# Performance work log

Measured on AMD Instinct MI355X. Metric: run time of the kernel, lower is better.

## Reference

```python
import jax, jax.numpy as jnp
import numpy as np

HIDDEN = 1024
N_HEAD = 16
D_HEAD = HIDDEN // N_HEAD


def setup_inputs() -> dict:
    key = jax.random.key(0)
    ks = jax.random.split(key, 12)
    B, S, H = 2, 2048, HIDDEN
    scale = 1.0 / np.sqrt(H)
    inp = {
        "q": jax.random.normal(ks[0], (B, S, H), jnp.float32),
        "k": jax.random.normal(ks[1], (B, S, H), jnp.float32),
        "v": jax.random.normal(ks[2], (B, S, H), jnp.float32),
        "mask": jnp.ones((B, 1, S, S), jnp.int32),
        "w_q": jax.random.normal(ks[3], (H, H), jnp.float32) * scale,
        "b_q": jnp.zeros((H,), jnp.float32),
        "w_k": jax.random.normal(ks[4], (H, H), jnp.float32) * scale,
        "b_k": jnp.zeros((H,), jnp.float32),
        "w_v": jax.random.normal(ks[5], (H, H), jnp.float32) * scale,
        "b_v": jnp.zeros((H,), jnp.float32),
        "w_o": jax.random.normal(ks[6], (H, H), jnp.float32) * scale,
        "b_o": jnp.zeros((H,), jnp.float32),
    }
    return inp


def reference(q, k, v, mask, w_q, b_q, w_k, b_k, w_v, b_v, w_o, b_o):
    B, Sq, H = q.shape
    Sk = k.shape[1]
    # projections (weights stored as [in, out])
    qh = (q @ w_q + b_q).reshape(B, Sq, N_HEAD, D_HEAD).transpose(0, 2, 1, 3)
    kh = (k @ w_k + b_k).reshape(B, Sk, N_HEAD, D_HEAD).transpose(0, 2, 1, 3)
    vh = (v @ w_v + b_v).reshape(B, Sk, N_HEAD, D_HEAD).transpose(0, 2, 1, 3)
    scores = jnp.einsum("bhqd,bhkd->bhqk", qh, kh) * (D_HEAD ** -0.5)
    scores = jnp.where(mask == 0, jnp.float32(-10000.0), scores)
    attn = jax.nn.softmax(scores, axis=-1)
    out = jnp.einsum("bhqk,bhkd->bhqd", attn, vh)
    out = out.transpose(0, 2, 1, 3).reshape(B, Sq, H)
    return out @ w_o + b_o
```

## Files before the change

kernel.cpp:

```cpp
#include <hip/hip_runtime.h>
#include <hip/hip_bf16.h>
#include <stdint.h>

#define S_LEN 2048
#define HID   1024
#define NHEAD 16
#define DHEAD 64
#define BATCH 2

#define QSCALE 0.18033688f
#define MASKNEG -14427.0f

typedef __bf16 bf16_t;
typedef __bf16 bf16x4 __attribute__((ext_vector_type(4)));
typedef __bf16 bf16x8 __attribute__((ext_vector_type(8)));
typedef float  f32x4  __attribute__((ext_vector_type(4)));


__device__ __forceinline__ void gl_lds16(const bf16_t* g, bf16_t* l) {
  __builtin_amdgcn_global_load_lds((const __attribute__((address_space(1))) void*)g,
                                   (__attribute__((address_space(3))) void*)l,
                                   16, 0, 0);
}

template<int TR, int TC>
__device__ __forceinline__ void stage_tile(const bf16_t* __restrict__ g, int ldg,
                                           bf16_t* lds, int wave, int lane) {
  constexpr int CH = TC / 8;
  constexpr int NINST = (TR * CH) / 64;
  #pragma unroll
  for (int i = wave; i < NINST; i += 4) {
    int slot = i * 64 + lane;
    int r  = slot / CH;
    int cs = slot & (CH - 1);
    int c  = cs ^ (r & (CH - 1));
    gl_lds16(g + (size_t)r * ldg + c * 8, lds + i * 512);
  }
}

template<int CH>
__device__ __forceinline__ bf16x8 frag_ld(const bf16_t* lds, int row, int kchunk) {
  int cs = kchunk ^ (row & (CH - 1));
  return *(const bf16x8*)(lds + (row * CH + cs) * 8);
}

__global__ __launch_bounds__(256) void cvt3(const float* __restrict__ q,
                                            const float* __restrict__ k,
                                            const float* __restrict__ v,
                                            bf16_t* __restrict__ qb,
                                            bf16_t* __restrict__ kb,
                                            bf16_t* __restrict__ vb) {
  int which = blockIdx.y;
  const float* src = which == 0 ? q : which == 1 ? k : v;
  bf16_t* dst = which == 0 ? qb : which == 1 ? kb : vb;
  size_t i = ((size_t)blockIdx.x * 256 + threadIdx.x) * 4;
  float4 u = *(const float4*)(src + i);
  bf16x4 o = {(bf16_t)u.x, (bf16_t)u.y, (bf16_t)u.z, (bf16_t)u.w};
  *(bf16x4*)(dst + i) = o;
}

__global__ __launch_bounds__(256) void transpose_w4(
    const float* __restrict__ w0, const float* __restrict__ w1,
    const float* __restrict__ w2, const float* __restrict__ w3,
    bf16_t* __restrict__ wt, int* __restrict__ flags) {
  if (blockIdx.x == 0 && blockIdx.y == 0 && blockIdx.z == 0) {
    flags[threadIdx.x] = -1;
    flags[threadIdx.x + 256] = -1;
  }
  __shared__ float t[64][65];
  const float* W = blockIdx.z == 0 ? w0 : blockIdx.z == 1 ? w1 : blockIdx.z == 2 ? w2 : w3;
  bf16_t* WT = wt + (size_t)blockIdx.z * HID * HID;
  int tx = threadIdx.x & 63, ty = threadIdx.x >> 6;
  int r0 = blockIdx.y * 64, c0 = blockIdx.x * 64;
  #pragma unroll
  for (int i = ty; i < 64; i += 4) t[i][tx] = W[(size_t)(r0 + i) * HID + c0 + tx];
  __syncthreads();
  #pragma unroll
  for (int i = ty; i < 64; i += 4) WT[(size_t)(c0 + i) * HID + r0 + tx] = (bf16_t)t[tx][i];
}

__global__ __launch_bounds__(256) void mask_flags(const int* __restrict__ mask,
                                                  int* __restrict__ flags) {
  int qtile = blockIdx.x, rg = blockIdx.y, b = blockIdx.z;
  const int* base = mask + (size_t)b * S_LEN * S_LEN
                  + (size_t)(qtile * 128 + rg * 16) * S_LEN;
  int tid = threadIdx.x;
  int kt = tid >> 4;
  int ok = 1;
  #pragma unroll
  for (int r = 0; r < 16; ++r) {
    const int4* p = (const int4*)(base + (size_t)r * S_LEN + tid * 8);
    int4 a = p[0], c = p[1];
    ok &= (a.x != 0) & (a.y != 0) & (a.z != 0) & (a.w != 0) &
          (c.x != 0) & (c.y != 0) & (c.z != 0) & (c.w != 0);
  }
  __shared__ int oks[16];
  if (tid < 16) oks[tid] = -1;
  __syncthreads();
  if (!ok) atomicAnd(&oks[kt], 0);
  __syncthreads();
  if (tid < 16 && oks[tid] == 0) atomicAnd(&flags[(b * 16 + qtile) * 16 + tid], 0);
}

__global__ __launch_bounds__(256) void qkv_gemm(
    const bf16_t* __restrict__ qb, const bf16_t* __restrict__ kb, const bf16_t* __restrict__ vb,
    const bf16_t* __restrict__ wT,
    const float* __restrict__ bq, const float* __restrict__ bk, const float* __restrict__ bv,
    bf16_t* __restrict__ Qh, bf16_t* __restrict__ Kh, bf16_t* __restrict__ VhT) {
  int mode = blockIdx.z;
  const bf16_t* A    = mode == 0 ? qb : mode == 1 ? kb : vb;
  const bf16_t* Bt   = wT + (size_t)mode * HID * HID;
  const float*  bias = mode == 0 ? bq : mode == 1 ? bk : bv;

  __shared__ __align__(16) bf16_t As[128 * 64];
  __shared__ __align__(16) bf16_t Bs[128 * 64];

  int tid = threadIdx.x, wave = tid >> 6, lane = tid & 63;
  int lane15 = lane & 15, quad = lane >> 4;
  int m0 = blockIdx.x * 128, n0 = blockIdx.y * 128;
  int wm = (wave >> 1) * 64, wn = (wave & 1) * 64;

  f32x4 zero4 = {0.f, 0.f, 0.f, 0.f};
  f32x4 acc[4][4];
  #pragma unroll
  for (int t = 0; t < 4; ++t)
    #pragma unroll
    for (int n = 0; n < 4; ++n) acc[t][n] = zero4;

  for (int k0 = 0; k0 < HID; k0 += 64) {
    stage_tile<128, 64>(A  + (size_t)m0 * HID + k0, HID, As, wave, lane);
    stage_tile<128, 64>(Bt + (size_t)n0 * HID + k0, HID, Bs, wave, lane);
    __syncthreads();
    #pragma unroll
    for (int kc = 0; kc < 2; ++kc) {
      bf16x8 af[4], bfr[4];
      #pragma unroll
      for (int t = 0; t < 4; ++t) af[t]  = frag_ld<8>(As, wm + t * 16 + lane15, kc * 4 + quad);
      #pragma unroll
      for (int n = 0; n < 4; ++n) bfr[n] = frag_ld<8>(Bs, wn + n * 16 + lane15, kc * 4 + quad);
      if (mode < 2) {
        #pragma unroll
        for (int t = 0; t < 4; ++t)
          #pragma unroll
          for (int n = 0; n < 4; ++n)
            acc[t][n] = __builtin_amdgcn_mfma_f32_16x16x32_bf16(af[t], bfr[n], acc[t][n], 0, 0, 0);
      } else {
        #pragma unroll
        for (int t = 0; t < 4; ++t)
          #pragma unroll
          for (int n = 0; n < 4; ++n)
            acc[t][n] = __builtin_amdgcn_mfma_f32_16x16x32_bf16(bfr[n], af[t], acc[t][n], 0, 0, 0);
      }
    }
    __syncthreads();
  }

  if (mode < 2) {
    float sc = (mode == 0) ? QSCALE : 1.0f;
    bf16_t* dst = (mode == 0 ? Qh : Kh);
    #pragma unroll
    for (int t = 0; t < 4; ++t) {
      #pragma unroll
      for (int n = 0; n < 4; ++n) {
        int col = n0 + wn + n * 16 + lane15;
        float bb = bias[col];
        #pragma unroll
        for (int i = 0; i < 4; ++i) {
          int row = m0 + wm + t * 16 + quad * 4 + i;
          bf16_t o = (bf16_t)((acc[t][n][i] + bb) * sc);
          int b = row >> 11, s = row & 2047;
          int h = col >> 6,  d = col & 63;
          dst[((size_t)(b * NHEAD + h) * S_LEN + s) * DHEAD + d] = o;
        }
      }
    }
  } else {
    #pragma unroll
    for (int n = 0; n < 4; ++n) {
      int dbase = n0 + wn + n * 16 + quad * 4;
      float4 bb4 = *(const float4*)(bias + dbase);
      #pragma unroll
      for (int t = 0; t < 4; ++t) {
        int token = m0 + wm + t * 16 + lane15;
        int b = token >> 11, s = token & 2047;
        #pragma unroll
        for (int i = 0; i < 4; ++i) {
          int dg = dbase + i;
          int h = dg >> 6, d = dg & 63;
          float bb = i == 0 ? bb4.x : i == 1 ? bb4.y : i == 2 ? bb4.z : bb4.w;
          VhT[((size_t)(b * NHEAD + h) * DHEAD + d) * S_LEN + s] = (bf16_t)(acc[t][n][i] + bb);
        }
      }
    }
  }
}

__global__ __launch_bounds__(256) void attn_kernel(
    const bf16_t* __restrict__ Qh, const bf16_t* __restrict__ Kh, const bf16_t* __restrict__ VhT,
    const int* __restrict__ mask, const int* __restrict__ flags,
    bf16_t* __restrict__ OP, float* __restrict__ LP) {
  __shared__ __align__(16) bf16_t Ks[128 * 64];
  __shared__ __align__(16) bf16_t VTs[64 * 128];
  __shared__ __align__(16) bf16_t Ps[128 * 32];

  int tid = threadIdx.x, wave = tid >> 6, lane = tid & 63;
  int lane15 = lane & 15, quad = lane >> 4;
  int bh = blockIdx.y, b = bh >> 4;
  int qt = blockIdx.x;
  int half = blockIdx.z;
  int wrow = wave * 32;

  stage_tile<128, 64>(Qh + ((size_t)bh * S_LEN + qt * 128) * DHEAD, DHEAD, Ks, wave, lane);
  __syncthreads();
  bf16x8 qa[2][2];
  #pragma unroll
  for (int kc = 0; kc < 2; ++kc)
    #pragma unroll
    for (int nq = 0; nq < 2; ++nq)
      qa[kc][nq] = frag_ld<8>(Ks, wrow + nq * 16 + lane15, kc * 4 + quad);
  __syncthreads();

  f32x4 zero4 = {0.f, 0.f, 0.f, 0.f};
  f32x4 o_acc[2][4];
  float l_acc[2] = {0.f, 0.f};
  #pragma unroll
  for (int nq = 0; nq < 2; ++nq)
    #pragma unroll
    for (int mt = 0; mt < 4; ++mt) o_acc[nq][mt] = zero4;

  for (int ktl = 0; ktl < 8; ++ktl) {
    int kt = half * 8 + ktl;
    stage_tile<128, 64>(Kh + ((size_t)bh * S_LEN + kt * 128) * DHEAD, DHEAD, Ks, wave, lane);
    stage_tile<64, 128>(VhT + (size_t)bh * DHEAD * S_LEN + kt * 128, S_LEN, VTs, wave, lane);
    __syncthreads();
    bool masked = flags[(b * 16 + qt) * 16 + kt] == 0;

    #pragma unroll
    for (int qtr = 0; qtr < 4; ++qtr) {
      f32x4 sa[2][2];
      #pragma unroll
      for (int nq = 0; nq < 2; ++nq)
        #pragma unroll
        for (int mc = 0; mc < 2; ++mc) sa[nq][mc] = zero4;
      #pragma unroll
      for (int kc = 0; kc < 2; ++kc) {
        bf16x8 kf[2];
        #pragma unroll
        for (int mc = 0; mc < 2; ++mc)
          kf[mc] = frag_ld<8>(Ks, qtr * 32 + mc * 16 + lane15, kc * 4 + quad);
        #pragma unroll
        for (int nq = 0; nq < 2; ++nq)
          #pragma unroll
          for (int mc = 0; mc < 2; ++mc)
            sa[nq][mc] = __builtin_amdgcn_mfma_f32_16x16x32_bf16(kf[mc], qa[kc][nq], sa[nq][mc], 0, 0, 0);
      }

      if (masked) {
        #pragma unroll
        for (int nq = 0; nq < 2; ++nq)
          #pragma unroll
          for (int mc = 0; mc < 2; ++mc)
            #pragma unroll
            for (int i = 0; i < 4; ++i) {
              int q = qt * 128 + wrow + nq * 16 + lane15;
              int c = kt * 128 + qtr * 32 + mc * 16 + quad * 4 + i;
              if (mask[(size_t)b * S_LEN * S_LEN + (size_t)q * S_LEN + c] == 0)
                sa[nq][mc][i] = MASKNEG;
            }
      }

      #pragma unroll
      for (int nq = 0; nq < 2; ++nq) {
        int q = wrow + nq * 16 + lane15;
        #pragma unroll
        for (int mc = 0; mc < 2; ++mc) {
          float e0 = exp2f(sa[nq][mc][0]), e1 = exp2f(sa[nq][mc][1]);
          float e2 = exp2f(sa[nq][mc][2]), e3 = exp2f(sa[nq][mc][3]);
          l_acc[nq] += (e0 + e1) + (e2 + e3);
          bf16x4 pk = {(bf16_t)e0, (bf16_t)e1, (bf16_t)e2, (bf16_t)e3};
          int chunk = mc * 2 + (quad >> 1);
          int slot = chunk ^ (q & 3);
          *(bf16x4*)(Ps + q * 32 + slot * 8 + (quad & 1) * 4) = pk;
        }
      }

      bf16x8 vf[4], pf[2];
      #pragma unroll
      for (int mt = 0; mt < 4; ++mt)
        vf[mt] = frag_ld<16>(VTs, mt * 16 + lane15, qtr * 4 + quad);
      #pragma unroll
      for (int nq = 0; nq < 2; ++nq)
        pf[nq] = frag_ld<4>(Ps, wrow + nq * 16 + lane15, quad);
      #pragma unroll
      for (int nq = 0; nq < 2; ++nq)
        #pragma unroll
        for (int mt = 0; mt < 4; ++mt)
          o_acc[nq][mt] = __builtin_amdgcn_mfma_f32_16x16x32_bf16(vf[mt], pf[nq], o_acc[nq][mt], 0, 0, 0);
    }
    __syncthreads();
  }

  #pragma unroll
  for (int nq = 0; nq < 2; ++nq) {
    float lv = l_acc[nq];
    lv += __shfl_xor(lv, 16);
    lv += __shfl_xor(lv, 32);
    int s = qt * 128 + wrow + nq * 16 + lane15;
    size_t obase = (size_t)(half * 32 + bh) * S_LEN + s;
    #pragma unroll
    for (int mt = 0; mt < 4; ++mt) {
      bf16x4 ov = {(bf16_t)o_acc[nq][mt][0], (bf16_t)o_acc[nq][mt][1],
                   (bf16_t)o_acc[nq][mt][2], (bf16_t)o_acc[nq][mt][3]};
      *(bf16x4*)(OP + obase * 64 + mt * 16 + quad * 4) = ov;
    }
    if (quad == 0) LP[obase] = lv;
  }
}

__global__ __launch_bounds__(256) void oproj_gemm(
    const bf16_t* __restrict__ OP, const float* __restrict__ LP,
    const bf16_t* __restrict__ Bt, const float* __restrict__ bias,
    float* __restrict__ out) {
  __shared__ __align__(16) bf16_t As[128 * 64];
  __shared__ __align__(16) bf16_t Bs[128 * 64];

  int tid = threadIdx.x, wave = tid >> 6, lane = tid & 63;
  int lane15 = lane & 15, quad = lane >> 4;
  int m0 = blockIdx.x * 128, n0 = blockIdx.y * 128;
  int wm = (wave >> 1) * 64, wn = (wave & 1) * 64;

  f32x4 zero4 = {0.f, 0.f, 0.f, 0.f};
  f32x4 acc[4][4];
  #pragma unroll
  for (int t = 0; t < 4; ++t)
    #pragma unroll
    for (int n = 0; n < 4; ++n) acc[t][n] = zero4;

  size_t i0base[4];
  int cc8[4];
  #pragma unroll
  for (int i = 0; i < 4; ++i) {
    int slot = i * 256 + tid;
    int r  = slot >> 3;
    int cs = slot & 7;
    int c  = cs ^ (r & 7);
    int row = m0 + r;
    int b = row >> 11, s = row & 2047;
    i0base[i] = (size_t)(b * 16) * S_LEN + s;
    cc8[i] = c * 8;
  }

  bf16x8 op0[4], op1[4];
  float lsum[4];
  #pragma unroll
  for (int i = 0; i < 4; ++i) {
    size_t i0 = i0base[i];
    size_t i1 = i0 + (size_t)32 * S_LEN;
    op0[i] = *(const bf16x8*)(OP + i0 * 64 + cc8[i]);
    op1[i] = *(const bf16x8*)(OP + i1 * 64 + cc8[i]);
    lsum[i] = LP[i0] + LP[i1];
  }

  for (int it = 0; it < 16; ++it) {
    __syncthreads();
    #pragma unroll
    for (int i = 0; i < 4; ++i) {
      float inv = 1.0f / lsum[i];
      bf16x8 o;
      #pragma unroll
      for (int j = 0; j < 8; ++j)
        o[j] = (bf16_t)(((float)op0[i][j] + (float)op1[i][j]) * inv);
      *(bf16x8*)(As + (i * 256 + tid) * 8) = o;
    }
    stage_tile<128, 64>(Bt + (size_t)n0 * HID + it * 64, HID, Bs, wave, lane);
    __syncthreads();
    if (it < 15) {
      #pragma unroll
      for (int i = 0; i < 4; ++i) {
        size_t i0 = i0base[i] + (size_t)(it + 1) * S_LEN;
        size_t i1 = i0 + (size_t)32 * S_LEN;
        op0[i] = *(const bf16x8*)(OP + i0 * 64 + cc8[i]);
        op1[i] = *(const bf16x8*)(OP + i1 * 64 + cc8[i]);
        lsum[i] = LP[i0] + LP[i1];
      }
    }
    #pragma unroll
    for (int kc = 0; kc < 2; ++kc) {
      bf16x8 af[4], bfr[4];
      #pragma unroll
      for (int t = 0; t < 4; ++t) af[t]  = frag_ld<8>(As, wm + t * 16 + lane15, kc * 4 + quad);
      #pragma unroll
      for (int n = 0; n < 4; ++n) bfr[n] = frag_ld<8>(Bs, wn + n * 16 + lane15, kc * 4 + quad);
      #pragma unroll
      for (int t = 0; t < 4; ++t)
        #pragma unroll
        for (int n = 0; n < 4; ++n)
          acc[t][n] = __builtin_amdgcn_mfma_f32_16x16x32_bf16(af[t], bfr[n], acc[t][n], 0, 0, 0);
    }
  }

  #pragma unroll
  for (int t = 0; t < 4; ++t) {
    #pragma unroll
    for (int n = 0; n < 4; ++n) {
      int col = n0 + wn + n * 16 + lane15;
      float bb = bias[col];
      #pragma unroll
      for (int i = 0; i < 4; ++i) {
        int row = m0 + wm + t * 16 + quad * 4 + i;
        out[(size_t)row * HID + col] = acc[t][n][i] + bb;
      }
    }
  }
}

extern "C" void kernel_launch(void* const* d_in, const int* in_sizes, int n_in,
                              void* d_out, int out_size, void* d_ws, size_t ws_size,
                              hipStream_t stream) {
  (void)in_sizes; (void)n_in; (void)out_size; (void)ws_size;
  const float* q  = (const float*)d_in[0];
  const float* k  = (const float*)d_in[1];
  const float* v  = (const float*)d_in[2];
  const int*  mask = (const int*)d_in[3];
  const float* wq = (const float*)d_in[4];
  const float* bq = (const float*)d_in[5];
  const float* wk = (const float*)d_in[6];
  const float* bk = (const float*)d_in[7];
  const float* wv = (const float*)d_in[8];
  const float* bv = (const float*)d_in[9];
  const float* wo = (const float*)d_in[10];
  const float* bo = (const float*)d_in[11];

  char* ws = (char*)d_ws;
  bf16_t* wT    = (bf16_t*)(ws);
  bf16_t* Qh    = (bf16_t*)(ws + (8u  << 20));
  bf16_t* Kh    = (bf16_t*)(ws + (16u << 20));
  bf16_t* VhT   = (bf16_t*)(ws + (24u << 20));
  bf16_t* qb    = (bf16_t*)(ws + (32u << 20));
  bf16_t* kb    = (bf16_t*)(ws + (40u << 20));
  bf16_t* vb    = (bf16_t*)(ws + (48u << 20));
  int* flags    = (int*)(ws + (56u << 20));
  bf16_t* OP    = (bf16_t*)(ws + (32u << 20));
  float*  LPx   = (float*)(ws + (48u << 20));

  cvt3<<<dim3(4096, 3), 256, 0, stream>>>(q, k, v, qb, kb, vb);
  transpose_w4<<<dim3(16, 16, 4), 256, 0, stream>>>(wq, wk, wv, wo, wT, flags);
  mask_flags<<<dim3(16, 8, 2), 256, 0, stream>>>(mask, flags);
  qkv_gemm<<<dim3(32, 8, 3), 256, 0, stream>>>(qb, kb, vb, wT, bq, bk, bv, Qh, Kh, VhT);
  attn_kernel<<<dim3(16, 32, 2), 256, 0, stream>>>(Qh, Kh, VhT, mask, flags, OP, LPx);
  oproj_gemm<<<dim3(32, 8), 256, 0, stream>>>(OP, LPx, wT + (size_t)3 * HID * HID, bo, (float*)d_out);
}
```

Baseline: 297.7 us.

## Fuse fp32-to-bf16 conversion into QKV GEMM and split attention combine out of o-proj

Drops the separate cvt3 pass. The QKV GEMM now loads fp32 activations directly, converts them to bf16 in registers and stores them into swizzled LDS, prefetching the next k-tile while computing. This removes one full read/write pass of the bf16 copies, at the cost of twice the A-tile global traffic inside the GEMM and register staging instead of direct global-to-LDS loads. The split-attention combine, which the o-proj GEMM had been recomputing redundantly across its 8 column blocks, moves into its own small kernel. O-proj then uses plain direct LDS staging, which adds a launch and an extra buffer round-trip.

```diff
diff --git a/kernel.cpp b/kernel.cpp
--- a/kernel.cpp
+++ b/kernel.cpp
@@ -42,21 +42,6 @@
 __device__ __forceinline__ bf16x8 frag_ld(const bf16_t* lds, int row, int kchunk) {
   int cs = kchunk ^ (row & (CH - 1));
   return *(const bf16x8*)(lds + (row * CH + cs) * 8);
-}
-
-__global__ __launch_bounds__(256) void cvt3(const float* __restrict__ q,
-                                            const float* __restrict__ k,
-                                            const float* __restrict__ v,
-                                            bf16_t* __restrict__ qb,
-                                            bf16_t* __restrict__ kb,
-                                            bf16_t* __restrict__ vb) {
-  int which = blockIdx.y;
-  const float* src = which == 0 ? q : which == 1 ? k : v;
-  bf16_t* dst = which == 0 ? qb : which == 1 ? kb : vb;
-  size_t i = ((size_t)blockIdx.x * 256 + threadIdx.x) * 4;
-  float4 u = *(const float4*)(src + i);
-  bf16x4 o = {(bf16_t)u.x, (bf16_t)u.y, (bf16_t)u.z, (bf16_t)u.w};
-  *(bf16x4*)(dst + i) = o;
 }
 
 __global__ __launch_bounds__(256) void transpose_w4(
@@ -103,12 +88,12 @@
 }
 
 __global__ __launch_bounds__(256) void qkv_gemm(
-    const bf16_t* __restrict__ qb, const bf16_t* __restrict__ kb, const bf16_t* __restrict__ vb,
+    const float* __restrict__ qf, const float* __restrict__ kf32, const float* __restrict__ vf32,
     const bf16_t* __restrict__ wT,
     const float* __restrict__ bq, const float* __restrict__ bk, const float* __restrict__ bv,
     bf16_t* __restrict__ Qh, bf16_t* __restrict__ Kh, bf16_t* __restrict__ VhT) {
   int mode = blockIdx.z;
-  const bf16_t* A    = mode == 0 ? qb : mode == 1 ? kb : vb;
+  const float*  A    = mode == 0 ? qf : mode == 1 ? kf32 : vf32;
   const bf16_t* Bt   = wT + (size_t)mode * HID * HID;
   const float*  bias = mode == 0 ? bq : mode == 1 ? bk : bv;
 
@@ -127,10 +112,42 @@
     #pragma unroll
     for (int n = 0; n < 4; ++n) acc[t][n] = zero4;
 
-  for (int k0 = 0; k0 < HID; k0 += 64) {
-    stage_tile<128, 64>(A  + (size_t)m0 * HID + k0, HID, As, wave, lane);
+  const float* Abase = A + (size_t)m0 * HID;
+  int soff[4];
+  #pragma unroll
+  for (int i = 0; i < 4; ++i) {
+    int slot = i * 256 + tid;
+    int r = slot >> 3;
+    int c = (slot & 7) ^ (r & 7);
+    soff[i] = r * HID + c * 8;
+  }
+
+  float4 apre[4][2];
+  #pragma unroll
+  for (int i = 0; i < 4; ++i) {
+    const float4* src = (const float4*)(Abase + soff[i]);
+    apre[i][0] = src[0]; apre[i][1] = src[1];
+  }
+
+  for (int it = 0; it < 16; ++it) {
+    int k0 = it * 64;
+    __syncthreads();
+    #pragma unroll
+    for (int i = 0; i < 4; ++i) {
+      float4 u0 = apre[i][0], u1 = apre[i][1];
+      bf16x8 o = {(bf16_t)u0.x, (bf16_t)u0.y, (bf16_t)u0.z, (bf16_t)u0.w,
+                  (bf16_t)u1.x, (bf16_t)u1.y, (bf16_t)u1.z, (bf16_t)u1.w};
+      *(bf16x8*)(As + (i * 256 + tid) * 8) = o;
+    }
     stage_tile<128, 64>(Bt + (size_t)n0 * HID + k0, HID, Bs, wave, lane);
     __syncthreads();
+    if (it < 15) {
+      #pragma unroll
+      for (int i = 0; i < 4; ++i) {
+        const float4* src = (const float4*)(Abase + (k0 + 64) + soff[i]);
+        apre[i][0] = src[0]; apre[i][1] = src[1];
+      }
+    }
     #pragma unroll
     for (int kc = 0; kc < 2; ++kc) {
       bf16x8 af[4], bfr[4];
@@ -152,7 +169,6 @@
             acc[t][n] = __builtin_amdgcn_mfma_f32_16x16x32_bf16(bfr[n], af[t], acc[t][n], 0, 0, 0);
       }
     }
-    __syncthreads();
   }
 
   if (mode < 2) {
@@ -317,10 +333,27 @@
   }
 }
 
+__global__ __launch_bounds__(256) void attn_combine(
+    const bf16_t* __restrict__ OP, const float* __restrict__ LP,
+    bf16_t* __restrict__ O) {
+  int bh = blockIdx.y, b = bh >> 4, h = bh & 15;
+  int s = blockIdx.x * 32 + (threadIdx.x >> 3);
+  int d0 = (threadIdx.x & 7) * 8;
+  size_t i0 = (size_t)bh * S_LEN + s;
+  size_t i1 = (size_t)(32 + bh) * S_LEN + s;
+  bf16x8 a = *(const bf16x8*)(OP + i0 * 64 + d0);
+  bf16x8 c = *(const bf16x8*)(OP + i1 * 64 + d0);
+  float inv = 1.0f / (LP[i0] + LP[i1]);
+  bf16x8 o;
+  #pragma unroll
+  for (int j = 0; j < 8; ++j)
+    o[j] = (bf16_t)(((float)a[j] + (float)c[j]) * inv);
+  *(bf16x8*)(O + ((size_t)b * S_LEN + s) * HID + h * DHEAD + d0) = o;
+}
+
 __global__ __launch_bounds__(256) void oproj_gemm(
-    const bf16_t* __restrict__ OP, const float* __restrict__ LP,
-    const bf16_t* __restrict__ Bt, const float* __restrict__ bias,
-    float* __restrict__ out) {
+    const bf16_t* __restrict__ A, const bf16_t* __restrict__ Bt,
+    const float* __restrict__ bias, float* __restrict__ out) {
   __shared__ __align__(16) bf16_t As[128 * 64];
   __shared__ __align__(16) bf16_t Bs[128 * 64];
 
@@ -336,54 +369,10 @@
     #pragma unroll
     for (int n = 0; n < 4; ++n) acc[t][n] = zero4;
 
-  size_t i0base[4];
-  int cc8[4];
-  #pragma unroll
-  for (int i = 0; i < 4; ++i) {
-    int slot = i * 256 + tid;
-    int r  = slot >> 3;
-    int cs = slot & 7;
-    int c  = cs ^ (r & 7);
-    int row = m0 + r;
-    int b = row >> 11, s = row & 2047;
-    i0base[i] = (size_t)(b * 16) * S_LEN + s;
-    cc8[i] = c * 8;
-  }
-
-  bf16x8 op0[4], op1[4];
-  float lsum[4];
-  #pragma unroll
-  for (int i = 0; i < 4; ++i) {
-    size_t i0 = i0base[i];
-    size_t i1 = i0 + (size_t)32 * S_LEN;
-    op0[i] = *(const bf16x8*)(OP + i0 * 64 + cc8[i]);
-    op1[i] = *(const bf16x8*)(OP + i1 * 64 + cc8[i]);
-    lsum[i] = LP[i0] + LP[i1];
-  }
-
-  for (int it = 0; it < 16; ++it) {
-    __syncthreads();
-    #pragma unroll
-    for (int i = 0; i < 4; ++i) {
-      float inv = 1.0f / lsum[i];
-      bf16x8 o;
-      #pragma unroll
-      for (int j = 0; j < 8; ++j)
-        o[j] = (bf16_t)(((float)op0[i][j] + (float)op1[i][j]) * inv);
-      *(bf16x8*)(As + (i * 256 + tid) * 8) = o;
-    }
-    stage_tile<128, 64>(Bt + (size_t)n0 * HID + it * 64, HID, Bs, wave, lane);
-    __syncthreads();
-    if (it < 15) {
-      #pragma unroll
-      for (int i = 0; i < 4; ++i) {
-        size_t i0 = i0base[i] + (size_t)(it + 1) * S_LEN;
-        size_t i1 = i0 + (size_t)32 * S_LEN;
-        op0[i] = *(const bf16x8*)(OP + i0 * 64 + cc8[i]);
-        op1[i] = *(const bf16x8*)(OP + i1 * 64 + cc8[i]);
-        lsum[i] = LP[i0] + LP[i1];
-      }
-    }
+  for (int k0 = 0; k0 < HID; k0 += 64) {
+    stage_tile<128, 64>(A  + (size_t)m0 * HID + k0, HID, As, wave, lane);
+    stage_tile<128, 64>(Bt + (size_t)n0 * HID + k0, HID, Bs, wave, lane);
+    __syncthreads();
     #pragma unroll
     for (int kc = 0; kc < 2; ++kc) {
       bf16x8 af[4], bfr[4];
@@ -397,6 +386,7 @@
         for (int n = 0; n < 4; ++n)
           acc[t][n] = __builtin_amdgcn_mfma_f32_16x16x32_bf16(af[t], bfr[n], acc[t][n], 0, 0, 0);
     }
+    __syncthreads();
   }
 
   #pragma unroll
@@ -436,17 +426,15 @@
   bf16_t* Qh    = (bf16_t*)(ws + (8u  << 20));
   bf16_t* Kh    = (bf16_t*)(ws + (16u << 20));
   bf16_t* VhT   = (bf16_t*)(ws + (24u << 20));
-  bf16_t* qb    = (bf16_t*)(ws + (32u << 20));
-  bf16_t* kb    = (bf16_t*)(ws + (40u << 20));
-  bf16_t* vb    = (bf16_t*)(ws + (48u << 20));
-  int* flags    = (int*)(ws + (56u << 20));
   bf16_t* OP    = (bf16_t*)(ws + (32u << 20));
   float*  LPx   = (float*)(ws + (48u << 20));
-
-  cvt3<<<dim3(4096, 3), 256, 0, stream>>>(q, k, v, qb, kb, vb);
+  int* flags    = (int*)(ws + (56u << 20));
+  bf16_t* Obuf  = Qh;
+
   transpose_w4<<<dim3(16, 16, 4), 256, 0, stream>>>(wq, wk, wv, wo, wT, flags);
   mask_flags<<<dim3(16, 8, 2), 256, 0, stream>>>(mask, flags);
-  qkv_gemm<<<dim3(32, 8, 3), 256, 0, stream>>>(qb, kb, vb, wT, bq, bk, bv, Qh, Kh, VhT);
+  qkv_gemm<<<dim3(32, 8, 3), 256, 0, stream>>>(q, k, v, wT, bq, bk, bv, Qh, Kh, VhT);
   attn_kernel<<<dim3(16, 32, 2), 256, 0, stream>>>(Qh, Kh, VhT, mask, flags, OP, LPx);
-  oproj_gemm<<<dim3(32, 8), 256, 0, stream>>>(OP, LPx, wT + (size_t)3 * HID * HID, bo, (float*)d_out);
-}
+  attn_combine<<<dim3(64, 32), 256, 0, stream>>>(OP, LPx, Obuf);
+  oproj_gemm<<<dim3(32, 8), 256, 0, stream>>>(Obuf, wT + (size_t)3 * HID * HID, bo, (float*)d_out);
+}
```

Result: no change. 299.5 us (+0.6%).
